# Kernel tuning notes

Measured on AMD Instinct MI355X. Metric: run time of the kernel, lower is better.

The kernel has to match this reference:

```python
import jax, jax.numpy as jnp
import numpy as np

B, S, D = 4, 4096, 1024

def setup_inputs() -> dict:
    key = jax.random.key(0)
    ks = jax.random.split(key, 8)
    scale = 1.0 / np.sqrt(D)
    return {
        "inputs": jax.random.normal(ks[0], (B, S, D), dtype=jnp.float32),
        "context": jax.random.normal(ks[1], (B, S, D), dtype=jnp.float32),
        "Wq": jax.random.normal(ks[2], (D, D), dtype=jnp.float32) * scale,
        "bq": jnp.zeros((D,), dtype=jnp.float32),
        "Wk": jax.random.normal(ks[3], (D, D), dtype=jnp.float32) * scale,
        "bk": jnp.zeros((D,), dtype=jnp.float32),
        "Wv": jax.random.normal(ks[4], (D, D), dtype=jnp.float32) * scale,
        "bv": jnp.zeros((D,), dtype=jnp.float32),
        "Wo": jax.random.normal(ks[5], (D, D), dtype=jnp.float32) * scale,
        "bo": jnp.zeros((D,), dtype=jnp.float32),
    }

def reference(inputs, context, Wq, bq, Wk, bk, Wv, bv, Wo, bo):
    phi = lambda x: jax.nn.elu(x) + 1.0
    q_phi = phi(jnp.einsum("bsd,de->bse", inputs, Wq) + bq)   # [B,S,D]
    k_phi = phi(jnp.einsum("bsd,de->bse", context, Wk) + bk)  # [B,S,D]
    v = jnp.einsum("bsd,de->bse", context, Wv) + bv           # [B,S,D]
    kv = jnp.einsum("bsd,bse->bde", k_phi, v)                 # [B,D,D]
    k_sum = jnp.sum(k_phi, axis=1)                            # [B,D]
    z = 1.0 / (jnp.einsum("bsd,bd->bs", q_phi, k_sum)[..., None] + 1e-6)  # [B,S,1]
    out = jnp.einsum("bsd,bde->bse", q_phi, kv) * z           # [B,S,D]
    return jnp.einsum("bsd,de->bse", out, Wo) + bo + inputs
```

## Files before the change

kernel.cpp:

```cpp
#include <hip/hip_runtime.h>


typedef __bf16 bf16x8 __attribute__((ext_vector_type(8)));
typedef __bf16 bf16x4 __attribute__((ext_vector_type(4)));
typedef float  f32x4  __attribute__((ext_vector_type(4)));

#define GLOBAL_AS __attribute__((address_space(1)))
#define LDS_AS    __attribute__((address_space(3)))

#define SS 4096
#define DD 1024

__device__ __forceinline__ __bf16 f2bf(float f) {
  union { float f; unsigned u; } a; a.f = f;
  unsigned r = a.u + 0x7FFFu + ((a.u >> 16) & 1u);
  union { unsigned short s; __bf16 b; } o; o.s = (unsigned short)(r >> 16);
  return o.b;
}

__device__ __forceinline__ void async_load16(const void* g, void* l) {
  __builtin_amdgcn_global_load_lds((const GLOBAL_AS void*)g, (LDS_AS void*)l, 16, 0, 0);
}

template<int MODE>
__global__ __launch_bounds__(256)
void gemm_bt(const __bf16* __restrict__ Ag, const __bf16* __restrict__ Bg,
             void* __restrict__ Cg, void* __restrict__ Cg2,
             int N, int K, long sA, long sB, long sC,
             const float* __restrict__ bias, const float* __restrict__ bias2,
             const float* __restrict__ zvec,
             const float* __restrict__ resid)
{
  union SMem {
    struct { __bf16 As[128 * 64]; __bf16 Bs[128 * 64]; } s;
    __bf16 T[128 * 136];
  };
  __shared__ SMem sm;

  int bx = blockIdx.x, by = blockIdx.y;
  {
    const int gx = gridDim.x, gy = gridDim.y;
    if ((gy & 7) == 0) {
      const int f = by * gx + bx;
      const int j = f & 7;
      const int u = f >> 3;
      bx = u % gx;
      by = j * (gy >> 3) + u / gx;
    }
  }
  int bz = blockIdx.z;
  int k0beg = 0, k0end = K;
  if (MODE == 5) {
    const int split = bz & 3;
    bz >>= 2;
    k0beg = split * (K >> 2);
    k0end = k0beg + (K >> 2);
  }

  const int tid = threadIdx.x;
  const long m0 = (long)by * 128;
  const __bf16* A = Ag + m0 * K + bz * sA;
  const __bf16* B;
  if (MODE == 8) {
    const int b = (int)(m0 >> 12);
    B = Bg + (long)bx * 128 * K + (long)b * sB;
  } else {
    B = Bg + (long)bx * 128 * K + bz * sB;
  }

  const int srow = tid >> 3;
  const int gcc8 = ((tid & 7) ^ (srow & 7)) * 8;

  const int lane = tid & 63;
  const int wave = tid >> 6;
  const int wm   = (wave >> 1) * 64;
  const int wn   = (wave & 1) * 64;
  const int ln   = lane & 15;
  const int quad = lane >> 4;
  const int rk   = ln & 7;

  f32x4 acc[4][4];
  const f32x4 zero = {0.f, 0.f, 0.f, 0.f};
#pragma unroll
  for (int i = 0; i < 4; i++)
#pragma unroll
    for (int j = 0; j < 4; j++) acc[i][j] = zero;

  for (int k0 = k0beg; k0 < k0end; k0 += 64) {
#pragma unroll
    for (int p = 0; p < 4; p++) {
      async_load16(A + (long)(p * 32 + srow) * K + k0 + gcc8, sm.s.As + p * 2048 + tid * 8);
      async_load16(B + (long)(p * 32 + srow) * K + k0 + gcc8, sm.s.Bs + p * 2048 + tid * 8);
    }
    __syncthreads();

#pragma unroll
    for (int ksub = 0; ksub < 2; ksub++) {
      const int cc = (ksub * 4 + quad) ^ rk;
      bf16x8 af[4], bfr[4];
#pragma unroll
      for (int i = 0; i < 4; i++)
        af[i] = *(const bf16x8*)(sm.s.As + (wm + i * 16 + ln) * 64 + cc * 8);
#pragma unroll
      for (int j = 0; j < 4; j++)
        bfr[j] = *(const bf16x8*)(sm.s.Bs + (wn + j * 16 + ln) * 64 + cc * 8);
#pragma unroll
      for (int i = 0; i < 4; i++)
#pragma unroll
        for (int j = 0; j < 4; j++)
          acc[i][j] = __builtin_amdgcn_mfma_f32_16x16x32_bf16(af[i], bfr[j], acc[i][j], 0, 0, 0);
    }
    __syncthreads();
  }

  const int n0g = bx * 128;

  if (MODE == 6) {
    const bool isK = (n0g < 1024);
    const float* bb = isK ? bias : bias2;
    const int nb = isK ? n0g : (n0g - 1024);
#pragma unroll
    for (int i = 0; i < 4; i++)
#pragma unroll
      for (int j = 0; j < 4; j++)
#pragma unroll
        for (int r = 0; r < 4; r++) {
          const int s_loc = wm + i * 16 + quad * 4 + r;
          const int n_loc = wn + j * 16 + ln;
          float x = acc[i][j][r] + bb[nb + n_loc];
          if (isK) x = (x > 0.f) ? (x + 1.f) : __expf(x);
          sm.T[n_loc * 136 + s_loc] = f2bf(x);
        }
    __syncthreads();
    const int  b    = (int)(m0 >> 12);
    const long s_in = m0 & 4095;
    __bf16* dst = (__bf16*)(isK ? Cg : Cg2) + (long)b * DD * SS;
#pragma unroll
    for (int pass = 0; pass < 8; pass++) {
      const int row = (tid >> 4) + pass * 16;
      const int c   = (tid & 15) * 8;
      bf16x8 vv = *(const bf16x8*)(sm.T + row * 136 + c);
      *(bf16x8*)&dst[(long)(nb + row) * SS + s_in + c] = vv;
    }
    return;
  }

#pragma unroll
  for (int i = 0; i < 4; i++) {
#pragma unroll
    for (int j = 0; j < 4; j++) {
#pragma unroll
      for (int r = 0; r < 4; r++) {
        const int lrow = wm + i * 16 + quad * 4 + r;
        const int lcol = wn + j * 16 + ln;
        const long gm  = m0 + lrow;
        const int  gn  = n0g + lcol;
        float x = acc[i][j][r];
        if (MODE == 0) {
          x += bias[gn];
          x = (x > 0.f) ? (x + 1.f) : __expf(x);
          ((__bf16*)Cg)[gm * (long)N + gn] = f2bf(x);
        } else if (MODE == 5) {
          __hip_atomic_fetch_add(&((float*)Cg)[(long)bz * sC + gm * (long)N + gn],
                                 x, __ATOMIC_RELAXED, __HIP_MEMORY_SCOPE_AGENT);
        } else if (MODE == 7) {
          ((__bf16*)Cg)[(long)bz * sC + gm * (long)N + gn] = f2bf(x);
        } else if (MODE == 8) {
          x = x * zvec[gm] + bias[gn];
          ((float*)Cg)[gm * (long)N + gn] = x + resid[gm * (long)N + gn];
        }
      }
    }
  }
}

__global__ __launch_bounds__(256)
void cvt_f32_bf16(const float* __restrict__ x, __bf16* __restrict__ y, long n)
{
  long i = ((long)blockIdx.x * 256 + threadIdx.x) * 4;
  if (i < n) {
    float4 v = *(const float4*)(x + i);
    bf16x4 o;
    o[0] = f2bf(v.x); o[1] = f2bf(v.y); o[2] = f2bf(v.z); o[3] = f2bf(v.w);
    *(bf16x4*)(y + i) = o;
  }
}

__global__ __launch_bounds__(256)
void wtrans(const float* W0, const float* W1, const float* W2, const float* W3,
            __bf16* O0, __bf16* O1, __bf16* O2, __bf16* O3, int Dd)
{
  __shared__ __bf16 t[64][72];
  const float* W = (blockIdx.z == 0) ? W0 : (blockIdx.z == 1) ? W1 : (blockIdx.z == 2) ? W2 : W3;
  __bf16*      O = (blockIdx.z == 0) ? O0 : (blockIdx.z == 1) ? O1 : (blockIdx.z == 2) ? O2 : O3;
  const int r0 = blockIdx.y * 64, c0 = blockIdx.x * 64;
  const int tid = threadIdx.x;
  const int lr4 = tid >> 4, lc4 = (tid & 15) * 4;
#pragma unroll
  for (int it = 0; it < 4; it++) {
    const int row = lr4 + it * 16;
    float4 v = *(const float4*)&W[(long)(r0 + row) * Dd + c0 + lc4];
    t[row][lc4 + 0] = f2bf(v.x);
    t[row][lc4 + 1] = f2bf(v.y);
    t[row][lc4 + 2] = f2bf(v.z);
    t[row][lc4 + 3] = f2bf(v.w);
  }
  __syncthreads();
  const int lr8 = tid >> 3, lc8 = (tid & 7) * 8;
#pragma unroll
  for (int it = 0; it < 2; it++) {
    const int orow = lr8 + it * 32;
    bf16x8 vb;
#pragma unroll
    for (int j = 0; j < 8; j++) vb[j] = t[lc8 + j][orow];
    *(bf16x8*)&O[(long)(c0 + orow) * Dd + r0 + lc8] = vb;
  }
}

__global__ __launch_bounds__(256)
void ksum_k(const __bf16* __restrict__ kphiT, float* __restrict__ ksum, int S)
{
  const long row = blockIdx.x;
  const __bf16* p = kphiT + row * (long)S;
  const int tid = threadIdx.x;
  float s = 0.f;
  for (int j = tid * 8; j < S; j += 256 * 8) {
    bf16x8 v = *(const bf16x8*)&p[j];
#pragma unroll
    for (int e = 0; e < 8; e++) s += (float)v[e];
  }
  __shared__ float red[256];
  red[tid] = s; __syncthreads();
  for (int off = 128; off > 0; off >>= 1) {
    if (tid < off) red[tid] += red[tid + off];
    __syncthreads();
  }
  if (tid == 0) ksum[row] = red[0];
}

__global__ __launch_bounds__(256)
void zden_k(const __bf16* __restrict__ qphi, const float* __restrict__ ksum,
            float* __restrict__ z, int Dd, int S)
{
  const long row = blockIdx.x;
  const int  b   = (int)(row / S);
  const __bf16* q = qphi + row * (long)Dd;
  const float* ks = ksum + (long)b * Dd;
  const int tid = threadIdx.x;
  const int i = tid * 4;
  bf16x4 qv = *(const bf16x4*)&q[i];
  float4 kv4 = *(const float4*)&ks[i];
  float s = (float)qv[0] * kv4.x + (float)qv[1] * kv4.y +
            (float)qv[2] * kv4.z + (float)qv[3] * kv4.w;
  __shared__ float red[256];
  red[tid] = s; __syncthreads();
  for (int off = 128; off > 0; off >>= 1) {
    if (tid < off) red[tid] += red[tid + off];
    __syncthreads();
  }
  if (tid == 0) z[row] = 1.f / (red[0] + 1e-6f);
}

extern "C" void kernel_launch(void* const* d_in, const int* in_sizes, int n_in,
                              void* d_out, int out_size, void* d_ws, size_t ws_size,
                              hipStream_t stream)
{
  const float* inputs  = (const float*)d_in[0];
  const float* context = (const float*)d_in[1];
  const float* Wq = (const float*)d_in[2];
  const float* bq = (const float*)d_in[3];
  const float* Wk = (const float*)d_in[4];
  const float* bk = (const float*)d_in[5];
  const float* Wv = (const float*)d_in[6];
  const float* bv = (const float*)d_in[7];
  const float* Wo = (const float*)d_in[8];
  const float* bo = (const float*)d_in[9];
  float* out = (float*)d_out;

  const int Bn = 4;
  const long NSD = (long)Bn * SS * DD;
  const long MB = 1L << 20;

  char* ws = (char*)d_ws;
  __bf16* xbf   = (__bf16*)(ws + 0 * MB);
  __bf16* cbf   = (__bf16*)(ws + 32 * MB);
  __bf16* qphi  = (__bf16*)(ws + 64 * MB);
  __bf16* kphiT = (__bf16*)(ws + 96 * MB);
  __bf16* vT    = (__bf16*)(ws + 128 * MB);
  float*  kvf   = (float*)(ws + 160 * MB);
  __bf16* kvbf  = (__bf16*)(ws + 176 * MB);
  __bf16* M2T   = (__bf16*)(ws + 184 * MB);
  __bf16* WqT   = (__bf16*)(ws + 192 * MB);
  __bf16* WkT   = (__bf16*)(ws + 194 * MB);
  __bf16* WvT   = (__bf16*)(ws + 196 * MB);
  __bf16* WoT   = (__bf16*)(ws + 198 * MB);
  float*  ksum  = (float*)(ws + 200 * MB);
  float*  zbuf  = (float*)(ws + 201 * MB);

  cvt_f32_bf16<<<16384, 256, 0, stream>>>(inputs,  xbf, NSD);
  cvt_f32_bf16<<<16384, 256, 0, stream>>>(context, cbf, NSD);
  wtrans<<<dim3(16, 16, 4), 256, 0, stream>>>(Wq, Wk, Wv, Wo, WqT, WkT, WvT, WoT, DD);

  gemm_bt<0><<<dim3(8, 128, 1), 256, 0, stream>>>(xbf, WqT, qphi, nullptr,
      DD, DD, 0, 0, 0, bq, nullptr, nullptr, nullptr);

  gemm_bt<6><<<dim3(16, 128, 1), 256, 0, stream>>>(cbf, WkT, kphiT, vT,
      2048, DD, 0, 0, 0, bk, bv, nullptr, nullptr);

  ksum_k<<<4096, 256, 0, stream>>>(kphiT, ksum, SS);
  zden_k<<<16384, 256, 0, stream>>>(qphi, ksum, zbuf, DD, SS);

  hipMemsetAsync(kvf, 0, (size_t)Bn * DD * DD * sizeof(float), stream);
  gemm_bt<5><<<dim3(8, 8, 16), 256, 0, stream>>>(kphiT, vT, kvf, nullptr,
      DD, SS, (long)DD * SS, (long)DD * SS, (long)DD * DD,
      nullptr, nullptr, nullptr, nullptr);
  cvt_f32_bf16<<<4096, 256, 0, stream>>>(kvf, kvbf, (long)Bn * DD * DD);

  gemm_bt<7><<<dim3(8, 8, 4), 256, 0, stream>>>(WoT, kvbf, M2T, nullptr,
      DD, DD, 0, (long)DD * DD, (long)DD * DD, nullptr, nullptr, nullptr, nullptr);

  gemm_bt<8><<<dim3(8, 128, 1), 256, 0, stream>>>(qphi, M2T, out, nullptr,
      DD, DD, 0, (long)DD * DD, 0, bo, nullptr, zbuf, inputs);
}
```

Before: 518.9 us.

## Add 256x256 tiled GEMM with multi-phase async LDS pipelining for projections

Introduces a new 512-thread GEMM kernel with 256x256 output tiles and a double-buffered LDS ring that issues async global-to-LDS loads for the next k-slices while MFMAs run on the current ones. Wave priority is raised around the MFMA blocks. It replaces the 128x128 kernel for the Q projection, the fused K/V projection and the final output GEMM. The goal is more data reuse per tile and hiding global-memory latency. In exchange it uses much more LDS and many more registers, so occupancy drops, and the grids have fewer blocks, which may leave CUs underused.

After: 524.2 us. About the same (+1.0%).

```diff
diff --git a/kernel.cpp b/kernel.cpp
--- a/kernel.cpp
+++ b/kernel.cpp
@@ -22,20 +22,73 @@
   __builtin_amdgcn_global_load_lds((const GLOBAL_AS void*)g, (LDS_AS void*)l, 16, 0, 0);
 }
 
+
+#define LA0 0
+#define LA1 16384
+#define LB0 32768
+#define LB1 49152
+
+#define VMW(n)  asm volatile("s_waitcnt vmcnt(" #n ")" ::: "memory")
+#define SBAR()  asm volatile("s_barrier" ::: "memory")
+#define LGK0()  do { asm volatile("s_waitcnt lgkmcnt(0)" ::: "memory"); \
+                     __builtin_amdgcn_sched_barrier(0); } while (0)
+
+#define STG_A(BASE, mh, kt) do {                                              \
+    async_load16(Aa + (long)((mh)*64 + t6) * K + (kt)*64 + gc8,               \
+                 smem + (BASE) + (mh)*8192 + tid*8);                          \
+    async_load16(Aa + (long)(128 + (mh)*64 + t6) * K + (kt)*64 + gc8,         \
+                 smem + (BASE) + (mh)*8192 + 4096 + tid*8);                   \
+  } while (0)
+
+#define STG_B(BASE, nh, kt) do {                                              \
+    async_load16(Bb + (long)(tA*64 + (nh)*32 + t5) * K + (kt)*64 + gc8,       \
+                 smem + (BASE) + (nh)*8192 + tid*8);                          \
+    async_load16(Bb + (long)(128 + tA*64 + (nh)*32 + t5) * K + (kt)*64 + gc8, \
+                 smem + (BASE) + (nh)*8192 + 4096 + tid*8);                   \
+  } while (0)
+
+#define PHASE(AB, BB, mh, nh, STG, EXTRA_VM) do {                             \
+    EXTRA_VM;                                                                 \
+    bf16x8 afrag[4][2], bfrag[2][2];                                          \
+    _Pragma("unroll") for (int rr = 0; rr < 4; ++rr) {                        \
+      const int o = (AB) + (mh)*8192 + rr*1024 + aoff;                        \
+      afrag[rr][0] = *(const bf16x8*)(smem + o);                              \
+      afrag[rr][1] = *(const bf16x8*)(smem + (o ^ 32));                       \
+    }                                                                         \
+    _Pragma("unroll") for (int nn = 0; nn < 2; ++nn) {                        \
+      const int o = (BB) + (nh)*8192 + nn*1024 + boff;                        \
+      bfrag[nn][0] = *(const bf16x8*)(smem + o);                              \
+      bfrag[nn][1] = *(const bf16x8*)(smem + (o ^ 32));                       \
+    }                                                                         \
+    STG;                                                                      \
+    SBAR();                                                                   \
+    LGK0();                                                                   \
+    __builtin_amdgcn_s_setprio(1);                                            \
+    _Pragma("unroll") for (int rr = 0; rr < 4; ++rr)                          \
+    _Pragma("unroll") for (int nn = 0; nn < 2; ++nn) {                        \
+      acc[(mh)*4+rr][(nh)*2+nn] = __builtin_amdgcn_mfma_f32_16x16x32_bf16(    \
+          afrag[rr][0], bfrag[nn][0], acc[(mh)*4+rr][(nh)*2+nn], 0, 0, 0);    \
+      acc[(mh)*4+rr][(nh)*2+nn] = __builtin_amdgcn_mfma_f32_16x16x32_bf16(    \
+          afrag[rr][1], bfrag[nn][1], acc[(mh)*4+rr][(nh)*2+nn], 0, 0, 0);    \
+    }                                                                         \
+    __builtin_amdgcn_s_setprio(0);                                            \
+    SBAR();                                                                   \
+  } while (0)
+
 template<int MODE>
-__global__ __launch_bounds__(256)
-void gemm_bt(const __bf16* __restrict__ Ag, const __bf16* __restrict__ Bg,
+__global__ __launch_bounds__(512, 2)
+void gemm256(const __bf16* __restrict__ Ag, const __bf16* __restrict__ Bg,
              void* __restrict__ Cg, void* __restrict__ Cg2,
-             int N, int K, long sA, long sB, long sC,
+             int N, int K, long sB,
              const float* __restrict__ bias, const float* __restrict__ bias2,
-             const float* __restrict__ zvec,
-             const float* __restrict__ resid)
+             const float* __restrict__ zvec, const float* __restrict__ resid)
 {
   union SMem {
-    struct { __bf16 As[128 * 64]; __bf16 Bs[128 * 64]; } s;
-    __bf16 T[128 * 136];
+    __bf16 st[65536];
+    __bf16 T[256 * 136];
   };
   __shared__ SMem sm;
+  __bf16* smem = sm.st;
 
   int bx = blockIdx.x, by = blockIdx.y;
   {
@@ -48,6 +101,147 @@
       by = j * (gy >> 3) + u / gx;
     }
   }
+
+  const int tid  = threadIdx.x;
+  const int lane = tid & 63, wave = tid >> 6;
+  const int wm   = wave >> 2, wn = wave & 3;
+  const int ln   = lane & 15, quad = lane >> 4;
+  const int t6   = tid >> 3, tA = t6 >> 5, t5 = t6 & 31;
+  const int gc8  = ((tid & 7) ^ (t6 & 7)) * 8;
+  const int pco  = (quad ^ (ln & 7)) * 8;
+  const int aoff = (wm * 64 + ln) * 64 + pco;
+  const int boff = (wn * 32 + ln) * 64 + pco;
+
+  const long m0  = (long)by * 256;
+  const int  n0g = bx * 256;
+  const __bf16* Aa = Ag + m0 * K;
+  const __bf16* Bb = Bg + (long)bx * 256 * K +
+                     ((MODE == 8) ? (long)(m0 >> 12) * sB : 0);
+
+  f32x4 acc[8][4];
+  const f32x4 zero = {0.f, 0.f, 0.f, 0.f};
+#pragma unroll
+  for (int i = 0; i < 8; i++)
+#pragma unroll
+    for (int j = 0; j < 4; j++) acc[i][j] = zero;
+
+  STG_A(LA0, 0, 0); STG_B(LB0, 0, 0);
+  STG_A(LA0, 1, 0); STG_B(LB0, 1, 0);
+  STG_A(LA1, 0, 1); STG_B(LB1, 0, 1);
+  VMW(8);
+  SBAR();
+
+  const int niter = K >> 7;
+#pragma unroll 1
+  for (int i = 0; i < niter - 1; ++i) {
+    const int kb = i * 2;
+    PHASE(LA0, LB0, 0, 0, STG_A(LA1, 1, kb + 1), VMW(4));
+    PHASE(LA0, LB0, 0, 1, STG_B(LB1, 1, kb + 1), );
+    PHASE(LA0, LB0, 1, 0, STG_A(LA0, 0, kb + 2), );
+    PHASE(LA0, LB0, 1, 1, STG_B(LB0, 0, kb + 2), VMW(6));
+    PHASE(LA1, LB1, 0, 0, STG_A(LA0, 1, kb + 2), VMW(4));
+    PHASE(LA1, LB1, 0, 1, STG_B(LB0, 1, kb + 2), );
+    PHASE(LA1, LB1, 1, 0, STG_A(LA1, 0, kb + 3), );
+    PHASE(LA1, LB1, 1, 1, STG_B(LB1, 0, kb + 3), VMW(6));
+  }
+  {
+    const int kb = (niter - 1) * 2;
+    PHASE(LA0, LB0, 0, 0, STG_A(LA1, 1, kb + 1), VMW(4));
+    PHASE(LA0, LB0, 0, 1, STG_B(LB1, 1, kb + 1), );
+    PHASE(LA0, LB0, 1, 0, , );
+    PHASE(LA0, LB0, 1, 1, , VMW(0));
+    PHASE(LA1, LB1, 0, 0, , );
+    PHASE(LA1, LB1, 0, 1, , );
+    PHASE(LA1, LB1, 1, 0, , );
+    PHASE(LA1, LB1, 1, 1, , );
+  }
+
+  if (MODE == 6) {
+    const bool isK = (n0g < 1024);
+    const float* bb = isK ? bias : bias2;
+    const int nb = isK ? n0g : (n0g - 1024);
+    const int b = (int)(m0 >> 12);
+    const long s_in = m0 & 4095;
+    __bf16* dst = (__bf16*)(isK ? Cg : Cg2) + (long)b * DD * SS;
+#pragma unroll
+    for (int h = 0; h < 2; ++h) {
+      if (wm == h) {
+#pragma unroll
+        for (int mf = 0; mf < 8; ++mf)
+#pragma unroll
+          for (int nf = 0; nf < 4; ++nf)
+#pragma unroll
+            for (int r = 0; r < 4; ++r) {
+              const int sl = mf * 16 + quad * 4 + r;
+              const int nl = wn * 64 + nf * 16 + ln;
+              float x = acc[mf][nf][r] + bb[nb + nl];
+              if (isK) x = (x > 0.f) ? (x + 1.f) : __expf(x);
+              sm.T[nl * 136 + sl] = f2bf(x);
+            }
+      }
+      __syncthreads();
+#pragma unroll
+      for (int p2 = 0; p2 < 8; ++p2) {
+        const int row = (tid >> 4) + p2 * 32;
+        const int c   = (tid & 15) * 8;
+        bf16x8 vv = *(const bf16x8*)(sm.T + row * 136 + c);
+        *(bf16x8*)&dst[(long)(nb + row) * SS + s_in + h * 128 + c] = vv;
+      }
+      __syncthreads();
+    }
+    return;
+  }
+
+#pragma unroll
+  for (int mf = 0; mf < 8; ++mf)
+#pragma unroll
+    for (int nf = 0; nf < 4; ++nf)
+#pragma unroll
+      for (int r = 0; r < 4; ++r) {
+        const long gm = m0 + wm * 128 + mf * 16 + quad * 4 + r;
+        const int  gn = n0g + wn * 64 + nf * 16 + ln;
+        float x = acc[mf][nf][r];
+        if (MODE == 0) {
+          x += bias[gn];
+          x = (x > 0.f) ? (x + 1.f) : __expf(x);
+          ((__bf16*)Cg)[gm * (long)N + gn] = f2bf(x);
+        } else {
+          x = x * zvec[gm] + bias[gn];
+          ((float*)Cg)[gm * (long)N + gn] = x + resid[gm * (long)N + gn];
+        }
+      }
+}
+
+#undef PHASE
+#undef STG_A
+#undef STG_B
+
+template<int MODE>
+__global__ __launch_bounds__(256)
+void gemm_bt(const __bf16* __restrict__ Ag, const __bf16* __restrict__ Bg,
+             void* __restrict__ Cg, void* __restrict__ Cg2,
+             int N, int K, long sA, long sB, long sC,
+             const float* __restrict__ bias, const float* __restrict__ bias2,
+             const float* __restrict__ zvec,
+             const float* __restrict__ resid)
+{
+  union SMem {
+    struct { __bf16 As[128 * 64]; __bf16 Bs[128 * 64]; } s;
+    __bf16 T[128 * 136];
+  };
+  __shared__ SMem sm;
+
+  int bx = blockIdx.x, by = blockIdx.y;
+  {
+    const int gx = gridDim.x, gy = gridDim.y;
+    if ((gy & 7) == 0) {
+      const int f = by * gx + bx;
+      const int j = f & 7;
+      const int u = f >> 3;
+      bx = u % gx;
+      by = j * (gy >> 3) + u / gx;
+    }
+  }
   int bz = blockIdx.z;
   int k0beg = 0, k0end = K;
   if (MODE == 5) {
@@ -60,13 +254,7 @@
   const int tid = threadIdx.x;
   const long m0 = (long)by * 128;
   const __bf16* A = Ag + m0 * K + bz * sA;
-  const __bf16* B;
-  if (MODE == 8) {
-    const int b = (int)(m0 >> 12);
-    B = Bg + (long)bx * 128 * K + (long)b * sB;
-  } else {
-    B = Bg + (long)bx * 128 * K + bz * sB;
-  }
+  const __bf16* B = Bg + (long)bx * 128 * K + bz * sB;
 
   const int srow = tid >> 3;
   const int gcc8 = ((tid & 7) ^ (srow & 7)) * 8;
@@ -114,37 +302,6 @@
   }
 
   const int n0g = bx * 128;
-
-  if (MODE == 6) {
-    const bool isK = (n0g < 1024);
-    const float* bb = isK ? bias : bias2;
-    const int nb = isK ? n0g : (n0g - 1024);
-#pragma unroll
-    for (int i = 0; i < 4; i++)
-#pragma unroll
-      for (int j = 0; j < 4; j++)
-#pragma unroll
-        for (int r = 0; r < 4; r++) {
-          const int s_loc = wm + i * 16 + quad * 4 + r;
-          const int n_loc = wn + j * 16 + ln;
-          float x = acc[i][j][r] + bb[nb + n_loc];
-          if (isK) x = (x > 0.f) ? (x + 1.f) : __expf(x);
-          sm.T[n_loc * 136 + s_loc] = f2bf(x);
-        }
-    __syncthreads();
-    const int  b    = (int)(m0 >> 12);
-    const long s_in = m0 & 4095;
-    __bf16* dst = (__bf16*)(isK ? Cg : Cg2) + (long)b * DD * SS;
-#pragma unroll
-    for (int pass = 0; pass < 8; pass++) {
-      const int row = (tid >> 4) + pass * 16;
-      const int c   = (tid & 15) * 8;
-      bf16x8 vv = *(const bf16x8*)(sm.T + row * 136 + c);
-      *(bf16x8*)&dst[(long)(nb + row) * SS + s_in + c] = vv;
-    }
-    return;
-  }
-
 #pragma unroll
   for (int i = 0; i < 4; i++) {
 #pragma unroll
@@ -156,18 +313,11 @@
         const long gm  = m0 + lrow;
         const int  gn  = n0g + lcol;
         float x = acc[i][j][r];
-        if (MODE == 0) {
-          x += bias[gn];
-          x = (x > 0.f) ? (x + 1.f) : __expf(x);
-          ((__bf16*)Cg)[gm * (long)N + gn] = f2bf(x);
-        } else if (MODE == 5) {
+        if (MODE == 5) {
           __hip_atomic_fetch_add(&((float*)Cg)[(long)bz * sC + gm * (long)N + gn],
                                  x, __ATOMIC_RELAXED, __HIP_MEMORY_SCOPE_AGENT);
         } else if (MODE == 7) {
           ((__bf16*)Cg)[(long)bz * sC + gm * (long)N + gn] = f2bf(x);
-        } else if (MODE == 8) {
-          x = x * zvec[gm] + bias[gn];
-          ((float*)Cg)[gm * (long)N + gn] = x + resid[gm * (long)N + gn];
         }
       }
     }
@@ -301,11 +451,11 @@
   cvt_f32_bf16<<<16384, 256, 0, stream>>>(context, cbf, NSD);
   wtrans<<<dim3(16, 16, 4), 256, 0, stream>>>(Wq, Wk, Wv, Wo, WqT, WkT, WvT, WoT, DD);
 
-  gemm_bt<0><<<dim3(8, 128, 1), 256, 0, stream>>>(xbf, WqT, qphi, nullptr,
-      DD, DD, 0, 0, 0, bq, nullptr, nullptr, nullptr);
-
-  gemm_bt<6><<<dim3(16, 128, 1), 256, 0, stream>>>(cbf, WkT, kphiT, vT,
-      2048, DD, 0, 0, 0, bk, bv, nullptr, nullptr);
+  gemm256<0><<<dim3(4, 64), 512, 0, stream>>>(xbf, WqT, qphi, nullptr,
+      DD, DD, 0, bq, nullptr, nullptr, nullptr);
+
+  gemm256<6><<<dim3(8, 64), 512, 0, stream>>>(cbf, WkT, kphiT, vT,
+      2048, DD, 0, bk, bv, nullptr, nullptr);
 
   ksum_k<<<4096, 256, 0, stream>>>(kphiT, ksum, SS);
   zden_k<<<16384, 256, 0, stream>>>(qphi, ksum, zbuf, DD, SS);
@@ -319,6 +469,6 @@
   gemm_bt<7><<<dim3(8, 8, 4), 256, 0, stream>>>(WoT, kvbf, M2T, nullptr,
       DD, DD, 0, (long)DD * DD, (long)DD * DD, nullptr, nullptr, nullptr, nullptr);
 
-  gemm_bt<8><<<dim3(8, 128, 1), 256, 0, stream>>>(qphi, M2T, out, nullptr,
-      DD, DD, 0, (long)DD * DD, 0, bo, nullptr, zbuf, inputs);
-}
+  gemm256<8><<<dim3(4, 64), 512, 0, stream>>>(qphi, M2T, out, nullptr,
+      DD, DD, (long)DD * DD, bo, nullptr, zbuf, inputs);
+}
```
